# Performance work log

Measured on AMD Instinct MI355X. Metric: run time of the kernel, lower is better.

Reference implementation:

```python
import jax, jax.numpy as jnp
import numpy as np

N_QUBITS = 10
T_STEPS = 10
NDATA = 1024
DIM = 2 ** N_QUBITS
PI = float(np.pi)


def setup_inputs() -> dict:
    key = jax.random.key(0)
    k1, k2, k3, k4, k5 = jax.random.split(key, 5)
    # random complex amplitudes (normalized to unit states inside reference)
    inputs_re = jax.random.normal(k1, (NDATA, DIM), dtype=jnp.float32)
    inputs_im = jax.random.normal(k2, (NDATA, DIM), dtype=jnp.float32)
    # diffusion noise schedule diff_hs (t,) in (0,1]
    diff_hs = jax.random.uniform(k5, (T_STEPS,), dtype=jnp.float32, minval=0.1, maxval=1.0)
    # var_1 = diff_hs.repeat(3n) in torch == tile -> index k scaled by diff_hs[k % t]
    var_1 = jnp.tile(diff_hs, 3 * N_QUBITS)                                  # (3*n*t,)
    phis = (jax.random.uniform(k3, (NDATA, 3 * N_QUBITS * T_STEPS), dtype=jnp.float32)
            * (PI / 4.0) - (PI / 8.0)) * var_1[None, :]
    gs = (jax.random.uniform(k4, (NDATA, T_STEPS), dtype=jnp.float32) * 0.2 + 0.4) * diff_hs[None, :]
    return {"inputs_re": inputs_re, "inputs_im": inputs_im, "phis": phis, "gs": gs}


def _apply_1q(psi, M, i):
    """Apply per-sample 2x2 gate M (B,2,2) on qubit i (qubit 0 = MSB) to psi (B, 2**n)."""
    left = 2 ** i
    right = 2 ** (N_QUBITS - 1 - i)
    s = psi.reshape(NDATA, left, 2, right)
    s = jnp.einsum('bxy,bayc->baxc', M, s)
    return s.reshape(NDATA, DIM)


def _scramble(inputs_re, inputs_im, phis, gs):
    n, t = N_QUBITS, T_STEPS
    psi = (inputs_re + 1j * inputs_im).astype(jnp.complex64)
    psi = psi / jnp.linalg.norm(psi, axis=1, keepdims=True)  # unit input states

    # precompute sum_{i<j} z_i z_j per basis state for the diagonal RZZ product
    idx = jnp.arange(DIM)
    bits = (idx[:, None] >> jnp.arange(n - 1, -1, -1)[None, :]) & 1  # (DIM, n), qubit0=MSB
    z = 1.0 - 2.0 * bits.astype(jnp.float32)
    zsum = z.sum(axis=1)
    pairsum = 0.5 * (zsum ** 2 - n)                                   # (DIM,)
    inv = 1.0 / (2.0 * np.sqrt(float(n)))

    for tt in range(t):
        base = 3 * n * tt
        for i in range(n):
            a = phis[:, base + i]            # first RZ angle
            th = phis[:, base + n + i]       # RY angle
            b = phis[:, base + 2 * n + i]    # second RZ angle
            c = jnp.cos(0.5 * th).astype(jnp.complex64)
            s = jnp.sin(0.5 * th).astype(jnp.complex64)
            ea_m = jnp.exp(-0.5j * a); ea_p = jnp.exp(0.5j * a)
            eb_m = jnp.exp(-0.5j * b); eb_p = jnp.exp(0.5j * b)
            # M = RZ(b) @ RY(th) @ RZ(a), per sample (B,2,2)
            M = jnp.stack([
                jnp.stack([eb_m * c * ea_m, -eb_m * s * ea_p], axis=-1),
                jnp.stack([eb_p * s * ea_m,  eb_p * c * ea_p], axis=-1),
            ], axis=-2)
            psi = _apply_1q(psi, M, i)
        # all RZZ(i,j, theta) gates are diagonal with shared theta -> single fused phase
        theta = (gs[:, tt] * inv).astype(jnp.complex64)
        psi = psi * jnp.exp(-0.5j * theta[:, None] * pairsum[None, :])
    return psi


def reference(inputs_re, inputs_im, phis, gs):
    psi = _scramble(inputs_re, inputs_im, phis, gs)
    return jnp.stack([psi.real, psi.imag])  # (2, Ndata, 2**n) float32
```

## Files before the change

kernel.cpp:

```cpp
#include <hip/hip_runtime.h>

#define NQ 10
#define TS 10
#define DIM 1024
#define ND 1024

typedef _Float16 h4 __attribute__((ext_vector_type(4)));
typedef __fp16  p2 __attribute__((ext_vector_type(2)));
typedef float f4 __attribute__((ext_vector_type(4)));

__device__ __forceinline__ f4 mfma16(h4 a, h4 b, f4 c) {
    return __builtin_amdgcn_mfma_f32_16x16x16f16(a, b, c, 0, 0, 0);
}
__device__ __forceinline__ h4 cvt_h4(f4 x) {
    p2 lo = __builtin_amdgcn_cvt_pkrtz(x[0], x[1]);
    p2 hi = __builtin_amdgcn_cvt_pkrtz(x[2], x[3]);
    h4 r; r[0] = lo[0]; r[1] = lo[1]; r[2] = hi[0]; r[3] = hi[1];
    return r;
}
__device__ __forceinline__ float hsel(int ob, int ib, float cq, float sq) {
    return (ob == ib) ? cq : (ob ? sq : -sq);
}

__global__ __launch_bounds__(64, 1) void qsim_kernel(
    const float* __restrict__ re_in, const float* __restrict__ im_in,
    const float* __restrict__ phis, const float* __restrict__ gs,
    float* __restrict__ out)
{
    const int sample = blockIdx.x;
    const int lane = threadIdx.x;
    const int quad = lane >> 4;
    const int cc = lane & 15;
    const int c3 = (cc >> 3) & 1, c2 = (cc >> 2) & 1, c1 = (cc >> 1) & 1, c0 = cc & 1;
    const int q1 = quad >> 1, q0 = quad & 1;

    const float* pr_in = re_in + sample * DIM;
    const float* pi_in = im_in + sample * DIM;
    const float* ph = phis + sample * (3 * NQ * TS);
    const float* gsp = gs + sample * TS;

    f4 Sr[4], Si[4];
    const int lbase = 256 * quad + cc;
#pragma unroll
    for (int n = 0; n < 4; ++n)
#pragma unroll
        for (int s = 0; s < 4; ++s) {
            Sr[n][s] = pr_in[lbase + 64 * s + 16 * n];
            Si[n][s] = pi_in[lbase + 64 * s + 16 * n];
        }

    const float inv = 0.15811388300841897f;
    float gk[TS];
#pragma unroll
    for (int t = 0; t < TS; ++t) gk[t] = -0.5f * (gsp[t] * inv);

    float nrm = 0.f;
#pragma unroll
    for (int n = 0; n < 4; ++n)
#pragma unroll
        for (int s = 0; s < 4; ++s) nrm += Sr[n][s] * Sr[n][s] + Si[n][s] * Si[n][s];
#pragma unroll
    for (int off = 32; off >= 1; off >>= 1) nrm += __shfl_xor(nrm, off, 64);
    const float scl = rsqrtf(nrm);
#pragma unroll
    for (int n = 0; n < 4; ++n) { Sr[n] *= scl; Si[n] *= scl; }

    float psv[4][4];
    const int pbase = __popc(quad) + __popc(cc);
#pragma unroll
    for (int n = 0; n < 4; ++n)
#pragma unroll
        for (int s = 0; s < 4; ++s) {
            const int p = pbase + __popc(n) + __popc(s);
            const int z = NQ - 2 * p;
            psv[n][s] = 0.5f * (float)(z * z - NQ);
        }
    const float fq1 = (float)q1, fq0 = (float)q0;
    const float fc3 = (float)c3, fc2 = (float)c2, fc1 = (float)c1, fc0 = (float)c0;

    float DCP[4][4], DSP[4][4];
    h4 gb; h4 hb[4][4];
    float bcur[NQ];

    auto make_trig = [&](const float* v, float kcur, float dcp[4][4], float dsp[4][4]) {
        float sv = 0.f;
#pragma unroll
        for (int i = 0; i < NQ; ++i) sv += v[i];
        float base = fmaf(-0.5f, sv, 0.f);
        base = fmaf(fq1, v[0], base); base = fmaf(fq0, v[1], base);
        base = fmaf(fc3, v[6], base); base = fmaf(fc2, v[7], base);
        base = fmaf(fc1, v[8], base); base = fmaf(fc0, v[9], base);
        const float addS[4] = {0.f, v[3], v[2], v[2] + v[3]};
        const float addN[4] = {0.f, v[5], v[4], v[4] + v[5]};
#pragma unroll
        for (int n = 0; n < 4; ++n)
#pragma unroll
            for (int s = 0; s < 4; ++s) {
                const float phi = fmaf(kcur, psv[n][s], base + addN[n] + addS[s]);
                dcp[n][s] = __cosf(phi);
                dsp[n][s] = __sinf(phi);
            }
    };
    auto make_tiles = [&](const float* th_src, h4& gbo, h4 hbo[4][4]) {
        float C[NQ], S[NQ];
#pragma unroll
        for (int g = 0; g < NQ; ++g) {
            const float h = 0.5f * th_src[g];
            S[g] = __sinf(h);
            C[g] = __cosf(h);
        }
        {
            const float f01 = hsel(c3, q1, C[0], S[0]) * hsel(c2, q0, C[1], S[1]);
            float e[4];
#pragma unroll
            for (int s = 0; s < 4; ++s)
                e[s] = f01 * hsel(c1, s >> 1, C[2], S[2]) * hsel(c0, s & 1, C[3], S[3]);
            p2 lo = __builtin_amdgcn_cvt_pkrtz(e[0], e[1]);
            p2 hi = __builtin_amdgcn_cvt_pkrtz(e[2], e[3]);
            gbo[0] = lo[0]; gbo[1] = lo[1]; gbo[2] = hi[0]; gbo[3] = hi[1];
        }
        const float F67 = hsel(c3, q1, C[6], S[6]) * hsel(c2, q0, C[7], S[7]);
        float F89[4];
#pragma unroll
        for (int s = 0; s < 4; ++s)
            F89[s] = F67 * hsel(c1, s >> 1, C[8], S[8]) * hsel(c0, s & 1, C[9], S[9]);
#pragma unroll
        for (int n = 0; n < 4; ++n)
#pragma unroll
            for (int j = 0; j < 4; ++j) {
                const float F45 = hsel(n >> 1, j >> 1, C[4], S[4])
                                * hsel(n & 1,  j & 1,  C[5], S[5]);
                p2 lo = __builtin_amdgcn_cvt_pkrtz(F45 * F89[0], F45 * F89[1]);
                p2 hi = __builtin_amdgcn_cvt_pkrtz(F45 * F89[2], F45 * F89[3]);
                hbo[n][j][0] = lo[0]; hbo[n][j][1] = lo[1];
                hbo[n][j][2] = hi[0]; hbo[n][j][3] = hi[1];
            }
    };

    {
        float phs[30];
#pragma unroll
        for (int j = 0; j < 30; ++j) phs[j] = ph[j];
        make_trig(&phs[0], 0.f, DCP, DSP);
        make_tiles(&phs[10], gb, hb);
#pragma unroll
        for (int i = 0; i < NQ; ++i) bcur[i] = phs[20 + i];
    }

    const f4 zf4 = {0.f, 0.f, 0.f, 0.f};

    for (int tt = 0; tt < TS; ++tt) {
#pragma unroll
        for (int n = 0; n < 4; ++n)
#pragma unroll
            for (int s = 0; s < 4; ++s) {
                const float cp = DCP[n][s], sp = DSP[n][s];
                const float xr = Sr[n][s], xi = Si[n][s];
                Sr[n][s] = cp * xr - sp * xi;
                Si[n][s] = sp * xr + cp * xi;
            }

        h4 gbN; h4 hbN[4][4];
        float DCPn[4][4], DSPn[4][4];
        float bnext[NQ];
        const bool last = (tt == TS - 1);
        {
            float phsN[30];
            if (!last) {
#pragma unroll
                for (int j = 0; j < 30; ++j) phsN[j] = ph[30 * (tt + 1) + j];
            } else {
#pragma unroll
                for (int j = 0; j < 30; ++j) phsN[j] = 0.f;
            }
            float vN[NQ];
#pragma unroll
            for (int i = 0; i < NQ; ++i) vN[i] = phsN[i] + bcur[i];
            make_trig(vN, gk[tt], DCPn, DSPn);
            if (!last) {
                make_tiles(&phsN[10], gbN, hbN);
#pragma unroll
                for (int i = 0; i < NQ; ++i) bnext[i] = phsN[20 + i];
            }
        }

        h4 ar[4], ai[4];
#pragma unroll
        for (int n = 0; n < 4; ++n) { ar[n] = cvt_h4(Sr[n]); ai[n] = cvt_h4(Si[n]); }
        f4 Tr[4], Ti[4];
#pragma unroll
        for (int n = 0; n < 4; ++n) {
            Tr[n] = mfma16(ar[n], gb, zf4);
            Ti[n] = mfma16(ai[n], gb, zf4);
        }
        h4 tr[4], ti[4];
#pragma unroll
        for (int n = 0; n < 4; ++n) { tr[n] = cvt_h4(Tr[n]); ti[n] = cvt_h4(Ti[n]); }
#pragma unroll
        for (int n = 0; n < 4; ++n) {
            f4 accr = zf4, acci = zf4;
#pragma unroll
            for (int j = 0; j < 4; ++j) {
                accr = mfma16(tr[j], hb[n][j], accr);
                acci = mfma16(ti[j], hb[n][j], acci);
            }
            Sr[n] = accr;
            Si[n] = acci;
        }

#pragma unroll
        for (int n = 0; n < 4; ++n)
#pragma unroll
            for (int s = 0; s < 4; ++s) { DCP[n][s] = DCPn[n][s]; DSP[n][s] = DSPn[n][s]; }
        if (!last) {
            gb = gbN;
#pragma unroll
            for (int n = 0; n < 4; ++n)
#pragma unroll
                for (int j = 0; j < 4; ++j) hb[n][j] = hbN[n][j];
#pragma unroll
            for (int i = 0; i < NQ; ++i) bcur[i] = bnext[i];
        }
    }

#pragma unroll
    for (int n = 0; n < 4; ++n)
#pragma unroll
        for (int s = 0; s < 4; ++s) {
            const float cp = DCP[n][s], sp = DSP[n][s];
            const float xr = Sr[n][s], xi = Si[n][s];
            Sr[n][s] = cp * xr - sp * xi;
            Si[n][s] = sp * xr + cp * xi;
        }

    float* outr = out + sample * DIM;
    float* outi = out + ND * DIM + sample * DIM;
#pragma unroll
    for (int n = 0; n < 4; ++n)
#pragma unroll
        for (int s = 0; s < 4; ++s) {
            outr[lbase + 64 * s + 16 * n] = Sr[n][s];
            outi[lbase + 64 * s + 16 * n] = Si[n][s];
        }
}

extern "C" void kernel_launch(void* const* d_in, const int* in_sizes, int n_in,
                              void* d_out, int out_size, void* d_ws, size_t ws_size,
                              hipStream_t stream) {
    const float* re_in = (const float*)d_in[0];
    const float* im_in = (const float*)d_in[1];
    const float* phis  = (const float*)d_in[2];
    const float* gs    = (const float*)d_in[3];
    float* out = (float*)d_out;
    qsim_kernel<<<ND, 64, 0, stream>>>(re_in, im_in, phis, gs, out);
}
```

Measured before the change: 80.02 us.

## Software-pipeline phase loads two steps ahead and fully unroll time loop

Phase angles are now prefetched two time steps ahead into a double-buffered register array. The trig and tile setup for the next step moves after the MFMA block and writes straight into the live arrays, removing the separate next-step copies. The time loop is fully unrolled so buffer indices resolve at compile time, and paired sin/cos calls are merged into sincos. The aim is to hide global-load latency and cut register pressure from duplicate state, at the cost of larger code size and a more serialized order of trig work and MFMA.

Result: faster. 77.90 us (-2.7%).

```diff
diff --git a/kernel.cpp b/kernel.cpp
--- a/kernel.cpp
+++ b/kernel.cpp
@@ -97,17 +97,19 @@
 #pragma unroll
             for (int s = 0; s < 4; ++s) {
                 const float phi = fmaf(kcur, psv[n][s], base + addN[n] + addS[s]);
-                dcp[n][s] = __cosf(phi);
-                dsp[n][s] = __sinf(phi);
+                float sp, cp;
+                __sincosf(phi, &sp, &cp);
+                dcp[n][s] = cp;
+                dsp[n][s] = sp;
             }
     };
     auto make_tiles = [&](const float* th_src, h4& gbo, h4 hbo[4][4]) {
         float C[NQ], S[NQ];
 #pragma unroll
         for (int g = 0; g < NQ; ++g) {
-            const float h = 0.5f * th_src[g];
-            S[g] = __sinf(h);
-            C[g] = __cosf(h);
+            float sg, cg;
+            __sincosf(0.5f * th_src[g], &sg, &cg);
+            S[g] = sg; C[g] = cg;
         }
         {
             const float f01 = hsel(c3, q1, C[0], S[0]) * hsel(c2, q0, C[1], S[1]);
@@ -138,17 +140,21 @@
     };
 
     {
-        float phs[30];
-#pragma unroll
-        for (int j = 0; j < 30; ++j) phs[j] = ph[j];
-        make_trig(&phs[0], 0.f, DCP, DSP);
-        make_tiles(&phs[10], gb, hb);
-#pragma unroll
-        for (int i = 0; i < NQ; ++i) bcur[i] = phs[20 + i];
+        float phs0[30];
+#pragma unroll
+        for (int j = 0; j < 30; ++j) phs0[j] = ph[j];
+        make_trig(&phs0[0], 0.f, DCP, DSP);
+        make_tiles(&phs0[10], gb, hb);
+#pragma unroll
+        for (int i = 0; i < NQ; ++i) bcur[i] = phs0[20 + i];
     }
+    float pipe[2][30];
+#pragma unroll
+    for (int j = 0; j < 30; ++j) pipe[0][j] = ph[30 + j];
 
     const f4 zf4 = {0.f, 0.f, 0.f, 0.f};
 
+#pragma unroll
     for (int tt = 0; tt < TS; ++tt) {
 #pragma unroll
         for (int n = 0; n < 4; ++n)
@@ -160,28 +166,9 @@
                 Si[n][s] = sp * xr + cp * xi;
             }
 
-        h4 gbN; h4 hbN[4][4];
-        float DCPn[4][4], DSPn[4][4];
-        float bnext[NQ];
-        const bool last = (tt == TS - 1);
-        {
-            float phsN[30];
-            if (!last) {
-#pragma unroll
-                for (int j = 0; j < 30; ++j) phsN[j] = ph[30 * (tt + 1) + j];
-            } else {
-#pragma unroll
-                for (int j = 0; j < 30; ++j) phsN[j] = 0.f;
-            }
-            float vN[NQ];
-#pragma unroll
-            for (int i = 0; i < NQ; ++i) vN[i] = phsN[i] + bcur[i];
-            make_trig(vN, gk[tt], DCPn, DSPn);
-            if (!last) {
-                make_tiles(&phsN[10], gbN, hbN);
-#pragma unroll
-                for (int i = 0; i < NQ; ++i) bnext[i] = phsN[20 + i];
-            }
+        if (tt + 2 < TS) {
+#pragma unroll
+            for (int j = 0; j < 30; ++j) pipe[(tt + 1) & 1][j] = ph[30 * (tt + 2) + j];
         }
 
         h4 ar[4], ai[4];
@@ -208,18 +195,17 @@
             Si[n] = acci;
         }
 
-#pragma unroll
-        for (int n = 0; n < 4; ++n)
-#pragma unroll
-            for (int s = 0; s < 4; ++s) { DCP[n][s] = DCPn[n][s]; DSP[n][s] = DSPn[n][s]; }
-        if (!last) {
-            gb = gbN;
-#pragma unroll
-            for (int n = 0; n < 4; ++n)
-#pragma unroll
-                for (int j = 0; j < 4; ++j) hb[n][j] = hbN[n][j];
-#pragma unroll
-            for (int i = 0; i < NQ; ++i) bcur[i] = bnext[i];
+        if (tt + 1 < TS) {
+            const float* pN = pipe[tt & 1];
+            float vN[NQ];
+#pragma unroll
+            for (int i = 0; i < NQ; ++i) vN[i] = pN[i] + bcur[i];
+            make_trig(vN, gk[tt], DCP, DSP);
+            make_tiles(&pN[10], gb, hb);
+#pragma unroll
+            for (int i = 0; i < NQ; ++i) bcur[i] = pN[20 + i];
+        } else {
+            make_trig(bcur, gk[TS - 1], DCP, DSP);
         }
     }
 
```
